# Kernel tuning notes

Hardware: AMD Instinct MI355X
Metric: run time of the kernel (lower is better)

Reference implementation:

```python
import jax, jax.numpy as jnp
import numpy as np

GRID_X, GRID_Y, GRID_Z = 200, 200, 8  # grid_size init kwarg (static)


def setup_inputs() -> dict:
    key = jax.random.key(0)
    k1, k2 = jax.random.split(key)
    B, N, D, H, W, C = 4, 6, 41, 16, 44, 64
    # ego-frame points roughly covering the grid extent [-50,50]x[-50,50]x[-4,4]
    scale = jnp.array([55.0, 55.0, 5.0], dtype=jnp.float32)
    geometry = jax.random.uniform(k1, (B, N, D, H, W, 3), dtype=jnp.float32,
                                  minval=-1.0, maxval=1.0) * scale
    features = jax.random.normal(k2, (B, N, D, H, W, C), dtype=jnp.float32)
    voxel_size = jnp.array([0.5, 0.5, 1.0], dtype=jnp.float32)
    voxel_origin = jnp.array([-50.0, -50.0, -4.0], dtype=jnp.float32)
    return {"geometry": geometry, "features": features,
            "voxel_size": voxel_size, "voxel_origin": voxel_origin}


def reference(geometry, features, voxel_size, voxel_origin):
    B = features.shape[0]
    C = features.shape[-1]
    pts = geometry.reshape(B, -1, 3)          # [B, P, 3]
    feat = features.reshape(B, -1, C)         # [B, P, C]

    # metric -> voxel index
    vi = jnp.floor((pts - voxel_origin) / voxel_size).astype(jnp.int32)  # [B, P, 3]
    x, y, z = vi[..., 0], vi[..., 1], vi[..., 2]
    valid = ((x >= 0) & (x < GRID_X) &
             (y >= 0) & (y < GRID_Y) &
             (z >= 0) & (z < GRID_Z))         # [B, P]

    # linear voxel index (z, x, y) ordering; invalid points scatter zeros to slot 0
    lin = z * (GRID_X * GRID_Y) + x * GRID_Y + y
    lin = jnp.where(valid, lin, 0)
    feat_m = jnp.where(valid[..., None], feat, 0.0)

    num_vox = GRID_Z * GRID_X * GRID_Y

    def pool_one(lin_b, feat_b):
        # scatter-add features into dense voxel grid: [num_vox, C]
        return jax.ops.segment_sum(feat_b, lin_b, num_segments=num_vox)

    vox = jax.vmap(pool_one)(lin, feat_m)                         # [B, num_vox, C]
    vox = vox.reshape(B, GRID_Z, GRID_X, GRID_Y, C)
    # torch.cat over z along channel dim => [B, Z*C, X, Y] with z-major blocks
    bev = jnp.transpose(vox, (0, 1, 4, 2, 3)).reshape(B, GRID_Z * C, GRID_X, GRID_Y)
    return bev
```

## Files before the change

kernel.cpp:

```cpp
#include <hip/hip_runtime.h>


#define GRID_X 200
#define GRID_Y 200
#define GRID_Z 8
#define NCH 64
#define NB 4
#define PTS_PER_BATCH (6 * 41 * 16 * 44)
#define TOTAL_POINTS (NB * PTS_PER_BATCH)
#define OUT_FLOATS ((long long)NB * GRID_Z * NCH * GRID_X * GRID_Y)

#define YT 2
#define TILE_Y 100
#define NBUCKET (NB * GRID_Z * GRID_X * YT)
#define NXCD 8
#define LDS_STRIDE 65

#define WS_CNT     0
#define WS_STARTS  (NBUCKET)
#define WS_CURSOR  (2 * NBUCKET + 1)
#define WS_SORTED  (3 * NBUCKET + 1)
#define WS_PCODE   (3 * NBUCKET + 1 + TOTAL_POINTS)
#define WS_INTS    (3 * NBUCKET + 1 + 2 * TOTAL_POINTS)

__device__ __forceinline__ bool point_voxel(const float* __restrict__ geom,
                                            const float* __restrict__ vsz,
                                            const float* __restrict__ vorg,
                                            int i, int& vx, int& vy, int& vz) {
    float px = geom[(size_t)i * 3 + 0];
    float py = geom[(size_t)i * 3 + 1];
    float pz = geom[(size_t)i * 3 + 2];
    vx = (int)floorf((px - vorg[0]) / vsz[0]);
    vy = (int)floorf((py - vorg[1]) / vsz[1]);
    vz = (int)floorf((pz - vorg[2]) / vsz[2]);
    return (vx >= 0 && vx < GRID_X && vy >= 0 && vy < GRID_Y &&
            vz >= 0 && vz < GRID_Z);
}

__global__ __launch_bounds__(256) void zero_cnt_kernel(int* __restrict__ cnt) {
    int i = blockIdx.x * 256 + threadIdx.x;
    if (i < NBUCKET) cnt[i] = 0;
}

__global__ __launch_bounds__(256) void hist_kernel(
    const float* __restrict__ geom, const float* __restrict__ vsz,
    const float* __restrict__ vorg, int* __restrict__ cnt,
    unsigned* __restrict__ pcode) {
    int i = blockIdx.x * 256 + threadIdx.x;
    if (i >= TOTAL_POINTS) return;
    int vx, vy, vz;
    unsigned code = 0;
    if (point_voxel(geom, vsz, vorg, i, vx, vy, vz)) {
        int b = i / PTS_PER_BATCH;
        int yt = vy / TILE_Y;
        int yl = vy - yt * TILE_Y;
        int bucket = ((b * GRID_Z + vz) * GRID_X + vx) * YT + yt;
        code = 0x80000000u | ((unsigned)yl << 14) | (unsigned)bucket;
        atomicAdd(&cnt[bucket], 1);
    }
    pcode[i] = code;
}

__global__ __launch_bounds__(256) void scan_kernel(
    const int* __restrict__ cnt, int* __restrict__ starts, int* __restrict__ cursor) {
    __shared__ int partial[256];
    int t = threadIdx.x;
    const int CHUNK = NBUCKET / 256;
    int base = t * CHUNK;
    int s = 0;
    for (int j = 0; j < CHUNK; ++j) s += cnt[base + j];
    partial[t] = s;
    __syncthreads();
    for (int off = 1; off < 256; off <<= 1) {
        int v = (t >= off) ? partial[t - off] : 0;
        __syncthreads();
        partial[t] += v;
        __syncthreads();
    }
    int run = partial[t] - s;
    for (int j = 0; j < CHUNK; ++j) {
        int c = cnt[base + j];
        starts[base + j] = run;
        cursor[base + j] = run;
        run += c;
    }
    if (t == 255) starts[NBUCKET] = run;
}

__global__ __launch_bounds__(256) void scatter_idx_kernel(
    const unsigned* __restrict__ pcode, int* __restrict__ cursor,
    unsigned* __restrict__ sorted) {
    int i = blockIdx.x * 256 + threadIdx.x;
    if (i >= TOTAL_POINTS) return;
    unsigned code = pcode[i];
    if (!(code & 0x80000000u)) return;
    int bucket = (int)(code & 0x3FFFu);
    unsigned yl = (code >> 14) & 0x7Fu;
    int pos = atomicAdd(&cursor[bucket], 1);
    sorted[pos] = (unsigned)i | (yl << 20);
}

__global__ __launch_bounds__(256) void pool_kernel(
    const float4* __restrict__ feat4, const unsigned* __restrict__ sorted,
    const int* __restrict__ starts, float4* __restrict__ out4) {
    __shared__ __align__(16) float acc[TILE_Y * LDS_STRIDE];
    int t = threadIdx.x;
    int bid = (blockIdx.x % NXCD) * (NBUCKET / NXCD) + blockIdx.x / NXCD;

    float4* a4 = (float4*)acc;
    for (int i = t; i < TILE_Y * LDS_STRIDE / 4; i += 256)
        a4[i] = make_float4(0.f, 0.f, 0.f, 0.f);
    __syncthreads();

    int s0 = starts[bid];
    int s1 = starts[bid + 1];
    int w = t >> 6;
    int g = (t >> 4) & 3;
    int l = t & 15;

    for (int p0 = s0 + w * 4; p0 < s1; p0 += 16) {
        int p = p0 + g;
        if (p < s1) {
            unsigned pk = sorted[p];
            unsigned idx = pk & 0xFFFFFu;
            unsigned yl = pk >> 20;
            float4 f = feat4[(size_t)idx * 16 + l];
            float* row = &acc[yl * LDS_STRIDE + 4 * l];
            atomicAdd(row + 0, f.x);
            atomicAdd(row + 1, f.y);
            atomicAdd(row + 2, f.z);
            atomicAdd(row + 3, f.w);
        }
    }
    __syncthreads();

    int yt = bid & 1;
    int x = (bid >> 1) % GRID_X;
    int bz = (bid >> 1) / GRID_X;

    for (int i = t; i < NCH * (TILE_Y / 4); i += 256) {
        int cc = i / (TILE_Y / 4);
        int j = i % (TILE_Y / 4);
        int y0 = 4 * j;
        float4 v = make_float4(acc[(y0 + 0) * LDS_STRIDE + cc],
                               acc[(y0 + 1) * LDS_STRIDE + cc],
                               acc[(y0 + 2) * LDS_STRIDE + cc],
                               acc[(y0 + 3) * LDS_STRIDE + cc]);
        size_t o4 = (((size_t)bz * NCH + cc) * GRID_X + x) * (GRID_Y / 4)
                    + yt * (TILE_Y / 4) + j;
        out4[o4] = v;
    }
}

__global__ __launch_bounds__(256) void zero_out_kernel(float4* __restrict__ out) {
    const long long n4 = OUT_FLOATS / 4;
    long long stride = (long long)gridDim.x * blockDim.x;
    for (long long i = blockIdx.x * (long long)blockDim.x + threadIdx.x;
         i < n4; i += stride)
        out[i] = make_float4(0.f, 0.f, 0.f, 0.f);
}

__global__ __launch_bounds__(256) void voxel_scatter_kernel(
    const float* __restrict__ geom, const float* __restrict__ feat,
    const float* __restrict__ vsz, const float* __restrict__ vorg,
    float* __restrict__ out) {
    int gid = blockIdx.x * blockDim.x + threadIdx.x;
    int pt = gid >> 6;
    int c = gid & 63;
    if (pt >= TOTAL_POINTS) return;
    int vx, vy, vz;
    if (!point_voxel(geom, vsz, vorg, pt, vx, vy, vz)) return;
    int b = pt / PTS_PER_BATCH;
    float f = feat[(size_t)pt * NCH + c];
    size_t idx = ((((size_t)b * GRID_Z + vz) * NCH + c) * GRID_X + vx) * GRID_Y + vy;
    atomicAdd(out + idx, f);
}

extern "C" void kernel_launch(void* const* d_in, const int* in_sizes, int n_in,
                              void* d_out, int out_size, void* d_ws, size_t ws_size,
                              hipStream_t stream) {
    const float* geom = (const float*)d_in[0];
    const float* feat = (const float*)d_in[1];
    const float* vsz  = (const float*)d_in[2];
    const float* vorg = (const float*)d_in[3];
    float* out = (float*)d_out;

    if (ws_size >= (size_t)WS_INTS * sizeof(int)) {
        int* ws = (int*)d_ws;
        int* cnt = ws + WS_CNT;
        int* starts = ws + WS_STARTS;
        int* cursor = ws + WS_CURSOR;
        unsigned* sorted = (unsigned*)(ws + WS_SORTED);
        unsigned* pcode  = (unsigned*)(ws + WS_PCODE);

        zero_cnt_kernel<<<(NBUCKET + 255) / 256, 256, 0, stream>>>(cnt);
        hist_kernel<<<TOTAL_POINTS / 256, 256, 0, stream>>>(geom, vsz, vorg, cnt, pcode);
        scan_kernel<<<1, 256, 0, stream>>>(cnt, starts, cursor);
        scatter_idx_kernel<<<TOTAL_POINTS / 256, 256, 0, stream>>>(pcode, cursor, sorted);
        pool_kernel<<<NBUCKET, 256, 0, stream>>>(
            (const float4*)feat, sorted, starts, (float4*)out);
    } else {
        zero_out_kernel<<<2048, 256, 0, stream>>>((float4*)out);
        const long long total_threads = (long long)TOTAL_POINTS * NCH;
        voxel_scatter_kernel<<<(int)((total_threads + 255) / 256), 256, 0, stream>>>(
            geom, feat, vsz, vorg, out);
    }
}
```

Before: 597.7 us.

## Split pooling into contiguous scratch write plus separate transpose kernel

Pooling now writes each bucket's channel-major tile contiguously into a workspace scratch buffer. A second kernel then copies those tiles into the final [B, Z*C, X, Y] layout with fully contiguous per-channel rows. The aim is to replace scattered 400-byte segment stores with contiguous streams. The cost is an extra full read and write of the output-sized buffer, and the path only runs when the workspace is large enough.

```diff
diff --git a/kernel.cpp b/kernel.cpp
--- a/kernel.cpp
+++ b/kernel.cpp
@@ -15,6 +15,7 @@
 #define NBUCKET (NB * GRID_Z * GRID_X * YT)
 #define NXCD 8
 #define LDS_STRIDE 65
+#define TILE_FLOATS (NCH * TILE_Y)
 
 #define WS_CNT     0
 #define WS_STARTS  (NBUCKET)
@@ -22,6 +23,8 @@
 #define WS_SORTED  (3 * NBUCKET + 1)
 #define WS_PCODE   (3 * NBUCKET + 1 + TOTAL_POINTS)
 #define WS_INTS    (3 * NBUCKET + 1 + 2 * TOTAL_POINTS)
+#define WS_SCRATCH ((WS_INTS + 3) & ~3)
+#define WS_INTS_2PH ((size_t)WS_SCRATCH + (size_t)NBUCKET * TILE_FLOATS)
 
 __device__ __forceinline__ bool point_voxel(const float* __restrict__ geom,
                                             const float* __restrict__ vsz,
@@ -100,7 +103,69 @@
     sorted[pos] = (unsigned)i | (yl << 20);
 }
 
-__global__ __launch_bounds__(256) void pool_kernel(
+__global__ __launch_bounds__(256) void pool_scratch_kernel(
+    const float4* __restrict__ feat4, const unsigned* __restrict__ sorted,
+    const int* __restrict__ starts, float4* __restrict__ scratch4) {
+    __shared__ __align__(16) float acc[TILE_Y * LDS_STRIDE];
+    int t = threadIdx.x;
+    int bid = blockIdx.x;
+
+    float4* a4 = (float4*)acc;
+    for (int i = t; i < TILE_Y * LDS_STRIDE / 4; i += 256)
+        a4[i] = make_float4(0.f, 0.f, 0.f, 0.f);
+    __syncthreads();
+
+    int s0 = starts[bid];
+    int s1 = starts[bid + 1];
+    int w = t >> 6;
+    int g = (t >> 4) & 3;
+    int l = t & 15;
+
+    for (int p0 = s0 + w * 4; p0 < s1; p0 += 16) {
+        int p = p0 + g;
+        if (p < s1) {
+            unsigned pk = sorted[p];
+            unsigned idx = pk & 0xFFFFFu;
+            unsigned yl = pk >> 20;
+            float4 f = feat4[(size_t)idx * 16 + l];
+            float* row = &acc[yl * LDS_STRIDE + 4 * l];
+            atomicAdd(row + 0, f.x);
+            atomicAdd(row + 1, f.y);
+            atomicAdd(row + 2, f.z);
+            atomicAdd(row + 3, f.w);
+        }
+    }
+    __syncthreads();
+
+    for (int i = t; i < TILE_FLOATS / 4; i += 256) {
+        int cc = i / (TILE_Y / 4);
+        int j = i % (TILE_Y / 4);
+        int y0 = 4 * j;
+        float4 v = make_float4(acc[(y0 + 0) * LDS_STRIDE + cc],
+                               acc[(y0 + 1) * LDS_STRIDE + cc],
+                               acc[(y0 + 2) * LDS_STRIDE + cc],
+                               acc[(y0 + 3) * LDS_STRIDE + cc]);
+        scratch4[(size_t)bid * (TILE_FLOATS / 4) + i] = v;
+    }
+}
+
+__global__ __launch_bounds__(256) void transpose_kernel(
+    const float4* __restrict__ scratch4, float4* __restrict__ out4) {
+    int t = threadIdx.x;
+    int cc = blockIdx.x & (NCH - 1);
+    int bz = blockIdx.x >> 6;
+    const size_t src_base = (size_t)bz * (GRID_X * YT) * (TILE_FLOATS / 4)
+                            + (size_t)cc * (TILE_Y / 4);
+    const size_t dst_base = ((size_t)bz * NCH + cc) * (GRID_X * GRID_Y / 4);
+    for (int i = t; i < GRID_X * GRID_Y / 4; i += 256) {
+        int seg = i / (TILE_Y / 4);
+        int j = i - seg * (TILE_Y / 4);
+        out4[dst_base + i] =
+            scratch4[src_base + (size_t)seg * (TILE_FLOATS / 4) + j];
+    }
+}
+
+__global__ __launch_bounds__(256) void pool_direct_kernel(
     const float4* __restrict__ feat4, const unsigned* __restrict__ sorted,
     const int* __restrict__ starts, float4* __restrict__ out4) {
     __shared__ __align__(16) float acc[TILE_Y * LDS_STRIDE];
@@ -197,8 +262,17 @@
         hist_kernel<<<TOTAL_POINTS / 256, 256, 0, stream>>>(geom, vsz, vorg, cnt, pcode);
         scan_kernel<<<1, 256, 0, stream>>>(cnt, starts, cursor);
         scatter_idx_kernel<<<TOTAL_POINTS / 256, 256, 0, stream>>>(pcode, cursor, sorted);
-        pool_kernel<<<NBUCKET, 256, 0, stream>>>(
-            (const float4*)feat, sorted, starts, (float4*)out);
+
+        if (ws_size >= WS_INTS_2PH * sizeof(int) + 16) {
+            float4* scratch4 = (float4*)(ws + WS_SCRATCH);
+            pool_scratch_kernel<<<NBUCKET, 256, 0, stream>>>(
+                (const float4*)feat, sorted, starts, scratch4);
+            transpose_kernel<<<NB * GRID_Z * NCH, 256, 0, stream>>>(
+                scratch4, (float4*)out);
+        } else {
+            pool_direct_kernel<<<NBUCKET, 256, 0, stream>>>(
+                (const float4*)feat, sorted, starts, (float4*)out);
+        }
     } else {
         zero_out_kernel<<<2048, 256, 0, stream>>>((float4*)out);
         const long long total_threads = (long long)TOTAL_POINTS * NCH;
```

Result: slower. 726.5 us (+21.5%).
